# Kernel optimization log

Hardware: AMD Instinct MI355X
Metric: run time of the kernel (lower is better)

Reference implementation:

```python
import jax, jax.numpy as jnp
import numpy as np
import math

N_TERMS = 10
TWO_PI = 2.0 * math.pi


def _zernike_tables(n_terms):
    # Terms in the exact order of the torch loops: n in [0,n_terms), m in range(-n, n+1, 2).
    terms = []
    for n in range(n_terms):
        for m in range(-n, n + 1, 2):
            terms.append((n, m))
    T = len(terms)  # n_terms*(n_terms+1)/2 = 55 for n_terms=10
    C = np.zeros((T, n_terms), dtype=np.float32)  # C[t, p] = coeff of rho**p for term t
    ms = np.zeros(T, dtype=np.float32)
    for t, (n, m) in enumerate(terms):
        am = abs(m)
        for k in range((n - am) // 2 + 1):
            c = ((-1) ** k) * math.factorial(n - k) / (
                math.factorial(k)
                * math.factorial((n + am) // 2 - k)
                * math.factorial((n - am) // 2 - k)
            )
            C[t, n - 2 * k] += c
        ms[t] = m
    return C, ms


_C_NP, _MS_NP = _zernike_tables(N_TERMS)


def setup_inputs() -> dict:
    key = jax.random.key(0)
    x = jax.random.normal(key, (32, 1, 1024, 1024), dtype=jnp.float32)
    return {"x": x}


def reference(x) -> jnp.ndarray:
    # FFT features
    fft_image = jnp.fft.rfft2(x)                    # [B,1,H,Wr], Wr = W//2+1
    magnitude = jnp.abs(fft_image)
    phase = jnp.angle(fft_image)
    pu = jnp.where(phase < 0, phase + TWO_PI, phase)  # "unwrapped" phase

    # Phase gradients (torch.gradient semantics == jnp.gradient: central diff, one-sided edges)
    grad_y, grad_x = jnp.gradient(pu, axis=(2, 3))

    # Zernike coefficients over the phase map grid
    B, _, H, Wr = pu.shape
    yv = jnp.linspace(-1.0, 1.0, H)
    xv = jnp.linspace(-1.0, 1.0, Wr)
    gy, gx = jnp.meshgrid(yv, xv, indexing="ij")   # [H,Wr]
    rho = jnp.sqrt(gx ** 2 + gy ** 2)
    theta = jnp.arctan2(gy, gx)
    mask = (rho <= 1.0).astype(pu.dtype)

    C = jnp.asarray(_C_NP)                          # [T,P]
    ms = jnp.asarray(_MS_NP)                        # [T]
    powers = jnp.arange(N_TERMS, dtype=pu.dtype)    # rho**0 .. rho**(n_terms-1)
    rho_pows = rho[None] ** powers[:, None, None]   # [P,H,Wr]
    R = jnp.einsum("tp,phw->thw", C, rho_pows)     # radial polynomials, [T,H,Wr]
    mt = ms[:, None, None] * theta[None]
    ang = jnp.where(ms[:, None, None] >= 0, jnp.cos(mt), jnp.sin(-mt))
    Z = R * ang                                     # [T,H,Wr]

    pm = pu[:, 0] * mask                            # [B,H,Wr]
    coeffs = jnp.einsum("bhw,thw->bt", pm, Z) / jnp.sum(mask)  # [B,T]

    # Slope stats (torch .std is unbiased -> ddof=1)
    slope_stats = jnp.concatenate(
        [
            grad_x.mean(axis=(2, 3)),
            grad_y.mean(axis=(2, 3)),
            grad_x.std(axis=(2, 3), ddof=1),
            grad_y.std(axis=(2, 3), ddof=1),
        ],
        axis=1,
    )                                               # [B,4]

    freq_features = jnp.max(magnitude, axis=(2, 3))  # [B,1]

    return jnp.concatenate([coeffs, slope_stats, freq_features], axis=1)  # [B,60]
```

## Files before the change

### kernel.cpp

```cpp
#include <hip/hip_runtime.h>
#include <math.h>

#define BATCH 32
#define HH 1024
#define WW 1024
#define WR 513
#define NPIX (HH * WR)
#define TWO_PI_F 6.28318530717958647692f

#define LGKM_SYNC() __asm__ __volatile__("s_waitcnt lgkmcnt(0)" ::: "memory")

__device__ __forceinline__ float2 cadd(float2 a, float2 b) { return make_float2(a.x + b.x, a.y + b.y); }
__device__ __forceinline__ float2 csub(float2 a, float2 b) { return make_float2(a.x - b.x, a.y - b.y); }
__device__ __forceinline__ float2 cmul(float2 a, float2 b) {
    return make_float2(a.x * b.x - a.y * b.y, a.x * b.y + a.y * b.x);
}

__device__ __forceinline__ float fast_atan2f(float y, float x) {
    float ax = __builtin_fabsf(x), ay = __builtin_fabsf(y);
    float mx = fmaxf(ax, ay), mn = fminf(ax, ay);
    float a = mn * __builtin_amdgcn_rcpf(mx);
    float s = a * a;
    float r = fmaf(fmaf(fmaf(fmaf(0.0208351f, s, -0.085133f), s, 0.180141f),
                        s, -0.3302995f), s, 0.999866f) * a;
    if (ay > ax) r = 1.5707963268f - r;
    if (x < 0.0f) r = 3.1415926536f - r;
    return (y < 0.0f) ? -r : r;
}

__device__ __forceinline__ void fft16(float2* d) {
    float2 b[16];
#pragma unroll
    for (int t = 0; t < 4; ++t) {
        float2 x0 = d[t], x1 = d[t + 4], x2 = d[t + 8], x3 = d[t + 12];
        float2 a0 = cadd(x0, x2), a1 = csub(x0, x2), a2 = cadd(x1, x3), a3 = csub(x1, x3);
        b[4 * t + 0] = cadd(a0, a2);
        b[4 * t + 1] = make_float2(a1.x + a3.y, a1.y - a3.x);
        b[4 * t + 2] = csub(a0, a2);
        b[4 * t + 3] = make_float2(a1.x - a3.y, a1.y + a3.x);
    }
    const float2 W1[4] = {make_float2(1.0f, 0.0f),
                          make_float2(0.92387953f, -0.38268343f),
                          make_float2(0.70710678f, -0.70710678f),
                          make_float2(0.38268343f, -0.92387953f)};
#pragma unroll
    for (int t = 0; t < 4; ++t) {
        float2 w1 = W1[t], w2 = cmul(w1, w1), w3 = cmul(w2, w1);
        float2 x0 = b[t], x1 = cmul(b[t + 4], w1), x2 = cmul(b[t + 8], w2), x3 = cmul(b[t + 12], w3);
        float2 a0 = cadd(x0, x2), a1 = csub(x0, x2), a2 = cadd(x1, x3), a3 = csub(x1, x3);
        d[t + 0]  = cadd(a0, a2);
        d[t + 4]  = make_float2(a1.x + a3.y, a1.y - a3.x);
        d[t + 8]  = csub(a0, a2);
        d[t + 12] = make_float2(a1.x - a3.y, a1.y + a3.x);
    }
}

__device__ __forceinline__ void wave_fft1024(float2* v, float* sb, int lane) {
    fft16(v);
    float s, c;
    __sincosf(-TWO_PI_F * (float)lane * (1.0f / 1024.0f), &s, &c);
    float2 T = make_float2(c, s), w = T;
#pragma unroll
    for (int k2 = 1; k2 < 16; ++k2) { v[k2] = cmul(v[k2], w); w = cmul(w, T); }
    const int k2p = lane & 15, qp = lane >> 4;
    float tx[16];
#pragma unroll
    for (int k2 = 0; k2 < 16; ++k2) sb[68 * k2 + lane] = v[k2].x;
    LGKM_SYNC();
#pragma unroll
    for (int m = 0; m < 16; ++m) tx[m] = sb[68 * k2p + 4 * m + qp];
    LGKM_SYNC();
#pragma unroll
    for (int k2 = 0; k2 < 16; ++k2) sb[68 * k2 + lane] = v[k2].y;
    LGKM_SYNC();
#pragma unroll
    for (int m = 0; m < 16; ++m) v[m] = make_float2(tx[m], sb[68 * k2p + 4 * m + qp]);
    LGKM_SYNC();
    fft16(v);
    __sincosf(-TWO_PI_F * (float)qp * (1.0f / 64.0f), &s, &c);
    float2 U = make_float2(c, s);
    w = U;
#pragma unroll
    for (int km = 1; km < 16; ++km) { v[km] = cmul(v[km], w); w = cmul(w, U); }
    const bool hi2 = (lane & 32) != 0, hi1 = (lane & 16) != 0;
#pragma unroll
    for (int m = 0; m < 16; ++m) {
        float2 a = v[m];
        float2 o = make_float2(__shfl_xor(a.x, 32, 64), __shfl_xor(a.y, 32, 64));
        float2 s1 = hi2 ? csub(o, a) : cadd(a, o);
        if (hi2 && hi1) s1 = make_float2(s1.y, -s1.x);
        float2 o2 = make_float2(__shfl_xor(s1.x, 16, 64), __shfl_xor(s1.y, 16, 64));
        v[m] = hi1 ? csub(o2, s1) : cadd(s1, o2);
    }
}

__global__ __launch_bounds__(256, 4) void row_fft_kernel(const float* __restrict__ x,
                                                         float2* __restrict__ rf2) {
    __shared__ float2 buf[4 * 1088];
    const int t = threadIdx.x, w = t >> 6, lane = t & 63;
    const int b = blockIdx.x >> 7;
    const int h0 = (blockIdx.x & 127) * 8;
    const float* r0 = x + ((long long)b * HH + h0 + 2 * w) * (long long)WW;
    const float* r1 = r0 + WW;
    float2 v[16];
#pragma unroll
    for (int j = 0; j < 16; ++j) v[j] = make_float2(r0[lane + 64 * j], r1[lane + 64 * j]);
    float2* mybuf = buf + w * 1088;
    wave_fft1024(v, (float*)mybuf, lane);
    const int kq = 2 * ((lane >> 4) & 1) + ((lane >> 5) & 1);
    const int kbase = (lane & 15) + 256 * kq;
#pragma unroll
    for (int m = 0; m < 16; ++m) mybuf[kbase + 16 * m] = v[m];
    __syncthreads();
    for (int idx = t; idx < 513 * 8; idx += 256) {
        int k = idx >> 3, j = idx & 7, p = j >> 1, which = j & 1;
        float2 zk = buf[p * 1088 + k];
        float2 zn = buf[p * 1088 + ((1024 - k) & 1023)];
        float2 val = which ? make_float2(0.5f * (zk.y + zn.y), 0.5f * (zn.x - zk.x))
                           : make_float2(0.5f * (zk.x + zn.x), 0.5f * (zk.y - zn.y));
        rf2[((long long)b * WR + k) * 1024 + h0 + j] = val;
    }
}

__global__ __launch_bounds__(128, 4) void col_fft_kernel(float2* __restrict__ rf2,
                                                         float* __restrict__ magmax) {
    __shared__ float sb[2 * 1088];
    const int t = threadIdx.x, w = t >> 6, lane = t & 63;
    const int fid = blockIdx.x * 2 + w;
    const int b = fid / WR, k = fid - b * WR;
    float2* row = rf2 + ((long long)b * WR + k) * 1024;
    float2 v[16];
#pragma unroll
    for (int j = 0; j < 16; ++j) v[j] = row[lane + 64 * j];
    wave_fft1024(v, sb + w * 1088, lane);
    float* pu = (float*)row;
    const int kq = 2 * ((lane >> 4) & 1) + ((lane >> 5) & 1);
    const int hbase = (lane & 15) + 256 * kq;
    float mmax = 0.0f;
#pragma unroll
    for (int m = 0; m < 16; ++m) {
        float2 z = v[m];
        mmax = fmaxf(mmax, __builtin_amdgcn_sqrtf(z.x * z.x + z.y * z.y));
        float ph = fast_atan2f(z.y, z.x);
        pu[hbase + 16 * m] = (ph < 0.0f) ? ph + TWO_PI_F : ph;
    }
#pragma unroll
    for (int off = 32; off; off >>= 1) mmax = fmaxf(mmax, __shfl_down(mmax, off));
    if (lane == 0) atomicMax((int*)(magmax + b), __float_as_int(mmax));
}

#define WRED(var, idx)                                                     \
    {                                                                      \
        float r_ = var;                                                    \
        _Pragma("unroll")                                                  \
        for (int off_ = 32; off_; off_ >>= 1) r_ += __shfl_down(r_, off_); \
        if (lane == 0) red[wv * 64 + (idx)] = r_;                          \
    }

__global__ __launch_bounds__(256, 2) void stats_kernel(float* __restrict__ pu) {
    __shared__ float red[4 * 64];
    const int b = blockIdx.y;
    const int k0 = blockIdx.x * 9;
    const float* base = pu + (long long)b * WR * 2048;
    float a00 = 0.f, a11 = 0.f, a20 = 0.f, a22 = 0.f, a31 = 0.f, a33 = 0.f,
          a40 = 0.f, a42 = 0.f, a44 = 0.f, a51 = 0.f, a53 = 0.f, a55 = 0.f,
          a60 = 0.f, a62 = 0.f, a64 = 0.f, a66 = 0.f, a71 = 0.f, a73 = 0.f,
          a75 = 0.f, a77 = 0.f, a80 = 0.f, a82 = 0.f, a84 = 0.f, a86 = 0.f,
          a88 = 0.f, a91 = 0.f, a93 = 0.f, a95 = 0.f, a97 = 0.f, a99 = 0.f;
    float b11 = 0.f, b22 = 0.f, b31 = 0.f, b33 = 0.f, b42 = 0.f, b44 = 0.f,
          b51 = 0.f, b53 = 0.f, b55 = 0.f, b62 = 0.f, b64 = 0.f, b66 = 0.f,
          b71 = 0.f, b73 = 0.f, b75 = 0.f, b77 = 0.f, b82 = 0.f, b84 = 0.f,
          b86 = 0.f, b88 = 0.f, b91 = 0.f, b93 = 0.f, b95 = 0.f, b97 = 0.f,
          b99 = 0.f;
    float sgx = 0.f, sgx2 = 0.f, sgy = 0.f, sgy2 = 0.f, cnt = 0.f;

    for (int kk = 0; kk < 9; ++kk) {
        const int k = k0 + kk;
        const float* rowc = base + (long long)k * 2048;
        const float* rowm = rowc - 2048;
        const float* rowp = rowc + 2048;
        const float xv = -1.0f + (1.0f / 256.0f) * (float)k;
        const float xv2 = xv * xv;
        for (int h = threadIdx.x; h < 1024; h += 256) {
            float v = rowc[h];
            float gx, gy;
            if (k == 0)            gx = rowp[h] - v;
            else if (k == WR - 1)  gx = v - rowm[h];
            else                   gx = 0.5f * (rowp[h] - rowm[h]);
            if (h == 0)            gy = rowc[1] - v;
            else if (h == 1023)    gy = v - rowc[1022];
            else                   gy = 0.5f * (rowc[h + 1] - rowc[h - 1]);
            sgx += gx; sgx2 += gx * gx; sgy += gy; sgy2 += gy * gy;

            const float yv = -1.0f + (2.0f / 1023.0f) * (float)h;
            const float r2 = xv2 + yv * yv;
            if (r2 <= 1.0f) {
                cnt += 1.0f;
                const float rho = sqrtf(r2);
                const float inv = rsqrtf(r2);
                const float c1 = xv * inv;
                const float s1 = yv * inv;
                const float c2 = 2.f * c1 * c1 - 1.f;
                const float c3 = 2.f * c1 * c2 - c1;
                const float c4 = 2.f * c1 * c3 - c2;
                const float c5 = 2.f * c1 * c4 - c3;
                const float c6 = 2.f * c1 * c5 - c4;
                const float c7 = 2.f * c1 * c6 - c5;
                const float c8 = 2.f * c1 * c7 - c6;
                const float c9 = 2.f * c1 * c8 - c7;
                const float s2 = 2.f * c1 * s1;
                const float s3 = 2.f * c1 * s2 - s1;
                const float s4 = 2.f * c1 * s3 - s2;
                const float s5 = 2.f * c1 * s4 - s3;
                const float s6 = 2.f * c1 * s5 - s4;
                const float s7 = 2.f * c1 * s6 - s5;
                const float s8 = 2.f * c1 * s7 - s6;
                const float s9 = 2.f * c1 * s8 - s7;
                const float w0 = v,        w1 = w0 * rho, w2 = w1 * rho, w3 = w2 * rho,
                            w4 = w3 * rho, w5 = w4 * rho, w6 = w5 * rho, w7 = w6 * rho,
                            w8 = w7 * rho, w9 = w8 * rho;
                a00 += w0;
                a11 += w1 * c1;
                a20 += w2;      a22 += w2 * c2;
                a31 += w3 * c1; a33 += w3 * c3;
                a40 += w4;      a42 += w4 * c2; a44 += w4 * c4;
                a51 += w5 * c1; a53 += w5 * c3; a55 += w5 * c5;
                a60 += w6;      a62 += w6 * c2; a64 += w6 * c4; a66 += w6 * c6;
                a71 += w7 * c1; a73 += w7 * c3; a75 += w7 * c5; a77 += w7 * c7;
                a80 += w8;      a82 += w8 * c2; a84 += w8 * c4; a86 += w8 * c6; a88 += w8 * c8;
                a91 += w9 * c1; a93 += w9 * c3; a95 += w9 * c5; a97 += w9 * c7; a99 += w9 * c9;
                b11 += w1 * s1;
                b22 += w2 * s2;
                b31 += w3 * s1; b33 += w3 * s3;
                b42 += w4 * s2; b44 += w4 * s4;
                b51 += w5 * s1; b53 += w5 * s3; b55 += w5 * s5;
                b62 += w6 * s2; b64 += w6 * s4; b66 += w6 * s6;
                b71 += w7 * s1; b73 += w7 * s3; b75 += w7 * s5; b77 += w7 * s7;
                b82 += w8 * s2; b84 += w8 * s4; b86 += w8 * s6; b88 += w8 * s8;
                b91 += w9 * s1; b93 += w9 * s3; b95 += w9 * s5; b97 += w9 * s7; b99 += w9 * s9;
            }
        }
    }

    const int wv = threadIdx.x >> 6, lane = threadIdx.x & 63;
    WRED(a00, 0);  WRED(a11, 1);  WRED(a20, 2);  WRED(a22, 3);  WRED(a31, 4);
    WRED(a33, 5);  WRED(a40, 6);  WRED(a42, 7);  WRED(a44, 8);  WRED(a51, 9);
    WRED(a53, 10); WRED(a55, 11); WRED(a60, 12); WRED(a62, 13); WRED(a64, 14);
    WRED(a66, 15); WRED(a71, 16); WRED(a73, 17); WRED(a75, 18); WRED(a77, 19);
    WRED(a80, 20); WRED(a82, 21); WRED(a84, 22); WRED(a86, 23); WRED(a88, 24);
    WRED(a91, 25); WRED(a93, 26); WRED(a95, 27); WRED(a97, 28); WRED(a99, 29);
    WRED(b11, 30); WRED(b22, 31); WRED(b31, 32); WRED(b33, 33); WRED(b42, 34);
    WRED(b44, 35); WRED(b51, 36); WRED(b53, 37); WRED(b55, 38); WRED(b62, 39);
    WRED(b64, 40); WRED(b66, 41); WRED(b71, 42); WRED(b73, 43); WRED(b75, 44);
    WRED(b77, 45); WRED(b82, 46); WRED(b84, 47); WRED(b86, 48); WRED(b88, 49);
    WRED(b91, 50); WRED(b93, 51); WRED(b95, 52); WRED(b97, 53); WRED(b99, 54);
    WRED(sgx, 55); WRED(sgx2, 56); WRED(sgy, 57); WRED(sgy2, 58); WRED(cnt, 59);
    __syncthreads();
    const int t = threadIdx.x;
    if (t < 60) {
        float s = red[t] + red[64 + t] + red[128 + t] + red[192 + t];
        pu[((long long)(b * 57 + blockIdx.x)) * 2048 + 1024 + t] = s;
    }
}

__device__ int moment_index(int p, int a, int is_cos) {
    int ai = 0;
    for (int pp = 0; pp < 10; ++pp)
        for (int aa = (pp & 1); aa <= pp; aa += 2) {
            if (is_cos && pp == p && aa == a) return ai;
            ++ai;
        }
    for (int pp = 1; pp < 10; ++pp)
        for (int aa = ((pp & 1) ? 1 : 2); aa <= pp; aa += 2) {
            if (!is_cos && pp == p && aa == a) return ai;
            ++ai;
        }
    return 0;
}

__device__ float factf(int n) {
    float f = 1.0f;
    for (int i = 2; i <= n; ++i) f *= (float)i;
    return f;
}

__global__ void finalize_kernel(const float* __restrict__ pu,
                                const float* __restrict__ magmax,
                                float* __restrict__ out) {
    __shared__ float abf[64];
    const int b = blockIdx.x;
    const int j = threadIdx.x;
    if (j < 60) {
        float s = 0.0f;
        for (int i = 0; i < 57; ++i)
            s += pu[((long long)(b * 57 + i)) * 2048 + 1024 + j];
        abf[j] = s;
    }
    __syncthreads();
    if (j >= 60) return;
    const float NF = (float)NPIX;
    float val;
    if (j < 55) {
        int tt = j, n = 0;
        while (tt >= n + 1) { tt -= (n + 1); ++n; }
        int m = -n + 2 * tt;
        int am = m < 0 ? -m : m;
        float s = 0.0f;
        for (int k = 0; k <= (n - am) / 2; ++k) {
            float c = factf(n - k) /
                      (factf(k) * factf((n + am) / 2 - k) * factf((n - am) / 2 - k));
            if (k & 1) c = -c;
            int p = n - 2 * k;
            s += c * abf[moment_index(p, am, m >= 0 ? 1 : 0)];
        }
        val = s / abf[59];
    } else if (j == 55) {
        val = abf[55] / NF;
    } else if (j == 56) {
        val = abf[57] / NF;
    } else if (j == 57) {
        float sum = abf[55], sq = abf[56];
        val = sqrtf(fmaxf(0.0f, (sq - sum * sum / NF) / (NF - 1.0f)));
    } else if (j == 58) {
        float sum = abf[57], sq = abf[58];
        val = sqrtf(fmaxf(0.0f, (sq - sum * sum / NF) / (NF - 1.0f)));
    } else {
        val = magmax[b];
    }
    out[b * 60 + j] = val;
}

extern "C" void kernel_launch(void* const* d_in, const int* in_sizes, int n_in,
                              void* d_out, int out_size, void* d_ws, size_t ws_size,
                              hipStream_t stream) {
    (void)in_sizes; (void)n_in; (void)out_size; (void)ws_size;
    const float* x = (const float*)d_in[0];
    float* out = (float*)d_out;

    float* magmax = (float*)d_ws;
    float2* rf2 = (float2*)((char*)d_ws + 16384);

    hipMemsetAsync(d_ws, 0, 16384, stream);
    row_fft_kernel<<<BATCH * 128, 256, 0, stream>>>(x, rf2);
    col_fft_kernel<<<(BATCH * WR) / 2, 128, 0, stream>>>(rf2, magmax);
    dim3 gridC(57, BATCH);
    stats_kernel<<<gridC, 256, 0, stream>>>((float*)rf2);
    finalize_kernel<<<BATCH, 64, 0, stream>>>((const float*)rf2, magmax, out);
}
```

Measured before the change: 509.1 us.

## Fuse Zernike moments and y-gradient stats into column FFT kernel

Computes the phase-map Zernike moments, y-gradient sums and mask count directly inside the column FFT kernel. The unwrapped phase is staged in padded shared memory and reduced per wave, and the per-row partials are written into the spare half of each row. The old stats kernel becomes a lighter float4-vectorized x-gradient kernel, and finalize sums 513 per-row partials instead of 57. This avoids re-reading the phase map for the moment computation but raises register pressure in the FFT kernel and makes finalize's serial loop longer.

```diff
diff --git a/kernel.cpp b/kernel.cpp
--- a/kernel.cpp
+++ b/kernel.cpp
@@ -9,6 +9,8 @@
 #define TWO_PI_F 6.28318530717958647692f
 
 #define LGKM_SYNC() __asm__ __volatile__("s_waitcnt lgkmcnt(0)" ::: "memory")
+
+#define PUIDX(h) ((h) + (((h) >> 8) << 3))
 
 __device__ __forceinline__ float2 cadd(float2 a, float2 b) { return make_float2(a.x + b.x, a.y + b.y); }
 __device__ __forceinline__ float2 csub(float2 a, float2 b) { return make_float2(a.x - b.x, a.y - b.y); }
@@ -132,7 +134,9 @@
     float2 v[16];
 #pragma unroll
     for (int j = 0; j < 16; ++j) v[j] = row[lane + 64 * j];
-    wave_fft1024(v, sb + w * 1088, lane);
+    float* mysb = sb + w * 1088;
+    wave_fft1024(v, mysb, lane);
+
     float* pu = (float*)row;
     const int kq = 2 * ((lane >> 4) & 1) + ((lane >> 5) & 1);
     const int hbase = (lane & 15) + 256 * kq;
@@ -142,26 +146,18 @@
         float2 z = v[m];
         mmax = fmaxf(mmax, __builtin_amdgcn_sqrtf(z.x * z.x + z.y * z.y));
         float ph = fast_atan2f(z.y, z.x);
-        pu[hbase + 16 * m] = (ph < 0.0f) ? ph + TWO_PI_F : ph;
+        float p = (ph < 0.0f) ? ph + TWO_PI_F : ph;
+        const int h = hbase + 16 * m;
+        pu[h] = p;
+        mysb[PUIDX(h)] = p;
     }
 #pragma unroll
     for (int off = 32; off; off >>= 1) mmax = fmaxf(mmax, __shfl_down(mmax, off));
     if (lane == 0) atomicMax((int*)(magmax + b), __float_as_int(mmax));
-}
-
-#define WRED(var, idx)                                                     \
-    {                                                                      \
-        float r_ = var;                                                    \
-        _Pragma("unroll")                                                  \
-        for (int off_ = 32; off_; off_ >>= 1) r_ += __shfl_down(r_, off_); \
-        if (lane == 0) red[wv * 64 + (idx)] = r_;                          \
-    }
-
-__global__ __launch_bounds__(256, 2) void stats_kernel(float* __restrict__ pu) {
-    __shared__ float red[4 * 64];
-    const int b = blockIdx.y;
-    const int k0 = blockIdx.x * 9;
-    const float* base = pu + (long long)b * WR * 2048;
+    LGKM_SYNC();
+
+    const float xv = -1.0f + (1.0f / 256.0f) * (float)k;
+    const float xv2 = xv * xv;
     float a00 = 0.f, a11 = 0.f, a20 = 0.f, a22 = 0.f, a31 = 0.f, a33 = 0.f,
           a40 = 0.f, a42 = 0.f, a44 = 0.f, a51 = 0.f, a53 = 0.f, a55 = 0.f,
           a60 = 0.f, a62 = 0.f, a64 = 0.f, a66 = 0.f, a71 = 0.f, a73 = 0.f,
@@ -172,94 +168,131 @@
           b71 = 0.f, b73 = 0.f, b75 = 0.f, b77 = 0.f, b82 = 0.f, b84 = 0.f,
           b86 = 0.f, b88 = 0.f, b91 = 0.f, b93 = 0.f, b95 = 0.f, b97 = 0.f,
           b99 = 0.f;
-    float sgx = 0.f, sgx2 = 0.f, sgy = 0.f, sgy2 = 0.f, cnt = 0.f;
-
+    float sgy = 0.f, sgy2 = 0.f, cnt = 0.f;
+
+#pragma unroll
+    for (int m = 0; m < 16; ++m) {
+        const int h = hbase + 16 * m;
+        const float v0 = mysb[PUIDX(h)];
+        float gy;
+        if (h == 0)         gy = mysb[PUIDX(1)] - v0;
+        else if (h == 1023) gy = v0 - mysb[PUIDX(1022)];
+        else                gy = 0.5f * (mysb[PUIDX(h + 1)] - mysb[PUIDX(h - 1)]);
+        sgy += gy; sgy2 += gy * gy;
+
+        const float yv = -1.0f + (2.0f / 1023.0f) * (float)h;
+        const float r2 = xv2 + yv * yv;
+        if (r2 <= 1.0f) {
+            cnt += 1.0f;
+            const float rho = sqrtf(r2);
+            const float inv = rsqrtf(r2);
+            const float c1 = xv * inv;
+            const float s1 = yv * inv;
+            const float c2 = 2.f * c1 * c1 - 1.f;
+            const float c3 = 2.f * c1 * c2 - c1;
+            const float c4 = 2.f * c1 * c3 - c2;
+            const float c5 = 2.f * c1 * c4 - c3;
+            const float c6 = 2.f * c1 * c5 - c4;
+            const float c7 = 2.f * c1 * c6 - c5;
+            const float c8 = 2.f * c1 * c7 - c6;
+            const float c9 = 2.f * c1 * c8 - c7;
+            const float s2 = 2.f * c1 * s1;
+            const float s3 = 2.f * c1 * s2 - s1;
+            const float s4 = 2.f * c1 * s3 - s2;
+            const float s5 = 2.f * c1 * s4 - s3;
+            const float s6 = 2.f * c1 * s5 - s4;
+            const float s7 = 2.f * c1 * s6 - s5;
+            const float s8 = 2.f * c1 * s7 - s6;
+            const float s9 = 2.f * c1 * s8 - s7;
+            const float w0 = v0,       w1 = w0 * rho, w2 = w1 * rho, w3 = w2 * rho,
+                        w4 = w3 * rho, w5 = w4 * rho, w6 = w5 * rho, w7 = w6 * rho,
+                        w8 = w7 * rho, w9 = w8 * rho;
+            a00 += w0;
+            a11 += w1 * c1;
+            a20 += w2;      a22 += w2 * c2;
+            a31 += w3 * c1; a33 += w3 * c3;
+            a40 += w4;      a42 += w4 * c2; a44 += w4 * c4;
+            a51 += w5 * c1; a53 += w5 * c3; a55 += w5 * c5;
+            a60 += w6;      a62 += w6 * c2; a64 += w6 * c4; a66 += w6 * c6;
+            a71 += w7 * c1; a73 += w7 * c3; a75 += w7 * c5; a77 += w7 * c7;
+            a80 += w8;      a82 += w8 * c2; a84 += w8 * c4; a86 += w8 * c6; a88 += w8 * c8;
+            a91 += w9 * c1; a93 += w9 * c3; a95 += w9 * c5; a97 += w9 * c7; a99 += w9 * c9;
+            b11 += w1 * s1;
+            b22 += w2 * s2;
+            b31 += w3 * s1; b33 += w3 * s3;
+            b42 += w4 * s2; b44 += w4 * s4;
+            b51 += w5 * s1; b53 += w5 * s3; b55 += w5 * s5;
+            b62 += w6 * s2; b64 += w6 * s4; b66 += w6 * s6;
+            b71 += w7 * s1; b73 += w7 * s3; b75 += w7 * s5; b77 += w7 * s7;
+            b82 += w8 * s2; b84 += w8 * s4; b86 += w8 * s6; b88 += w8 * s8;
+            b91 += w9 * s1; b93 += w9 * s3; b95 += w9 * s5; b97 += w9 * s7; b99 += w9 * s9;
+        }
+    }
+    LGKM_SYNC();
+
+#define CWRED(var, idx)                                                     \
+    {                                                                       \
+        float r_ = var;                                                     \
+        _Pragma("unroll")                                                   \
+        for (int off_ = 32; off_; off_ >>= 1) r_ += __shfl_down(r_, off_);  \
+        if (lane == 0) mysb[(idx)] = r_;                                    \
+    }
+    CWRED(a00, 0);  CWRED(a11, 1);  CWRED(a20, 2);  CWRED(a22, 3);  CWRED(a31, 4);
+    CWRED(a33, 5);  CWRED(a40, 6);  CWRED(a42, 7);  CWRED(a44, 8);  CWRED(a51, 9);
+    CWRED(a53, 10); CWRED(a55, 11); CWRED(a60, 12); CWRED(a62, 13); CWRED(a64, 14);
+    CWRED(a66, 15); CWRED(a71, 16); CWRED(a73, 17); CWRED(a75, 18); CWRED(a77, 19);
+    CWRED(a80, 20); CWRED(a82, 21); CWRED(a84, 22); CWRED(a86, 23); CWRED(a88, 24);
+    CWRED(a91, 25); CWRED(a93, 26); CWRED(a95, 27); CWRED(a97, 28); CWRED(a99, 29);
+    CWRED(b11, 30); CWRED(b22, 31); CWRED(b31, 32); CWRED(b33, 33); CWRED(b42, 34);
+    CWRED(b44, 35); CWRED(b51, 36); CWRED(b53, 37); CWRED(b55, 38); CWRED(b62, 39);
+    CWRED(b64, 40); CWRED(b66, 41); CWRED(b71, 42); CWRED(b73, 43); CWRED(b75, 44);
+    CWRED(b77, 45); CWRED(b82, 46); CWRED(b84, 47); CWRED(b86, 48); CWRED(b88, 49);
+    CWRED(b91, 50); CWRED(b93, 51); CWRED(b95, 52); CWRED(b97, 53); CWRED(b99, 54);
+    CWRED(sgy, 55); CWRED(sgy2, 56); CWRED(cnt, 57);
+#undef CWRED
+    LGKM_SYNC();
+    if (lane < 58) pu[1024 + lane] = mysb[lane];
+}
+
+__global__ __launch_bounds__(256, 2) void gx_kernel(float* __restrict__ pu) {
+    __shared__ float red[2 * 4];
+    const int b = blockIdx.y;
+    const int k0 = blockIdx.x * 9;
+    float* base = pu + (long long)b * WR * 2048;
+    const int t = threadIdx.x;
+    float sgx = 0.f, sgx2 = 0.f;
     for (int kk = 0; kk < 9; ++kk) {
         const int k = k0 + kk;
         const float* rowc = base + (long long)k * 2048;
-        const float* rowm = rowc - 2048;
-        const float* rowp = rowc + 2048;
-        const float xv = -1.0f + (1.0f / 256.0f) * (float)k;
-        const float xv2 = xv * xv;
-        for (int h = threadIdx.x; h < 1024; h += 256) {
-            float v = rowc[h];
-            float gx, gy;
-            if (k == 0)            gx = rowp[h] - v;
-            else if (k == WR - 1)  gx = v - rowm[h];
-            else                   gx = 0.5f * (rowp[h] - rowm[h]);
-            if (h == 0)            gy = rowc[1] - v;
-            else if (h == 1023)    gy = v - rowc[1022];
-            else                   gy = 0.5f * (rowc[h + 1] - rowc[h - 1]);
-            sgx += gx; sgx2 += gx * gx; sgy += gy; sgy2 += gy * gy;
-
-            const float yv = -1.0f + (2.0f / 1023.0f) * (float)h;
-            const float r2 = xv2 + yv * yv;
-            if (r2 <= 1.0f) {
-                cnt += 1.0f;
-                const float rho = sqrtf(r2);
-                const float inv = rsqrtf(r2);
-                const float c1 = xv * inv;
-                const float s1 = yv * inv;
-                const float c2 = 2.f * c1 * c1 - 1.f;
-                const float c3 = 2.f * c1 * c2 - c1;
-                const float c4 = 2.f * c1 * c3 - c2;
-                const float c5 = 2.f * c1 * c4 - c3;
-                const float c6 = 2.f * c1 * c5 - c4;
-                const float c7 = 2.f * c1 * c6 - c5;
-                const float c8 = 2.f * c1 * c7 - c6;
-                const float c9 = 2.f * c1 * c8 - c7;
-                const float s2 = 2.f * c1 * s1;
-                const float s3 = 2.f * c1 * s2 - s1;
-                const float s4 = 2.f * c1 * s3 - s2;
-                const float s5 = 2.f * c1 * s4 - s3;
-                const float s6 = 2.f * c1 * s5 - s4;
-                const float s7 = 2.f * c1 * s6 - s5;
-                const float s8 = 2.f * c1 * s7 - s6;
-                const float s9 = 2.f * c1 * s8 - s7;
-                const float w0 = v,        w1 = w0 * rho, w2 = w1 * rho, w3 = w2 * rho,
-                            w4 = w3 * rho, w5 = w4 * rho, w6 = w5 * rho, w7 = w6 * rho,
-                            w8 = w7 * rho, w9 = w8 * rho;
-                a00 += w0;
-                a11 += w1 * c1;
-                a20 += w2;      a22 += w2 * c2;
-                a31 += w3 * c1; a33 += w3 * c3;
-                a40 += w4;      a42 += w4 * c2; a44 += w4 * c4;
-                a51 += w5 * c1; a53 += w5 * c3; a55 += w5 * c5;
-                a60 += w6;      a62 += w6 * c2; a64 += w6 * c4; a66 += w6 * c6;
-                a71 += w7 * c1; a73 += w7 * c3; a75 += w7 * c5; a77 += w7 * c7;
-                a80 += w8;      a82 += w8 * c2; a84 += w8 * c4; a86 += w8 * c6; a88 += w8 * c8;
-                a91 += w9 * c1; a93 += w9 * c3; a95 += w9 * c5; a97 += w9 * c7; a99 += w9 * c9;
-                b11 += w1 * s1;
-                b22 += w2 * s2;
-                b31 += w3 * s1; b33 += w3 * s3;
-                b42 += w4 * s2; b44 += w4 * s4;
-                b51 += w5 * s1; b53 += w5 * s3; b55 += w5 * s5;
-                b62 += w6 * s2; b64 += w6 * s4; b66 += w6 * s6;
-                b71 += w7 * s1; b73 += w7 * s3; b75 += w7 * s5; b77 += w7 * s7;
-                b82 += w8 * s2; b84 += w8 * s4; b86 += w8 * s6; b88 += w8 * s8;
-                b91 += w9 * s1; b93 += w9 * s3; b95 += w9 * s5; b97 += w9 * s7; b99 += w9 * s9;
-            }
-        }
-    }
-
-    const int wv = threadIdx.x >> 6, lane = threadIdx.x & 63;
-    WRED(a00, 0);  WRED(a11, 1);  WRED(a20, 2);  WRED(a22, 3);  WRED(a31, 4);
-    WRED(a33, 5);  WRED(a40, 6);  WRED(a42, 7);  WRED(a44, 8);  WRED(a51, 9);
-    WRED(a53, 10); WRED(a55, 11); WRED(a60, 12); WRED(a62, 13); WRED(a64, 14);
-    WRED(a66, 15); WRED(a71, 16); WRED(a73, 17); WRED(a75, 18); WRED(a77, 19);
-    WRED(a80, 20); WRED(a82, 21); WRED(a84, 22); WRED(a86, 23); WRED(a88, 24);
-    WRED(a91, 25); WRED(a93, 26); WRED(a95, 27); WRED(a97, 28); WRED(a99, 29);
-    WRED(b11, 30); WRED(b22, 31); WRED(b31, 32); WRED(b33, 33); WRED(b42, 34);
-    WRED(b44, 35); WRED(b51, 36); WRED(b53, 37); WRED(b55, 38); WRED(b62, 39);
-    WRED(b64, 40); WRED(b66, 41); WRED(b71, 42); WRED(b73, 43); WRED(b75, 44);
-    WRED(b77, 45); WRED(b82, 46); WRED(b84, 47); WRED(b86, 48); WRED(b88, 49);
-    WRED(b91, 50); WRED(b93, 51); WRED(b95, 52); WRED(b97, 53); WRED(b99, 54);
-    WRED(sgx, 55); WRED(sgx2, 56); WRED(sgy, 57); WRED(sgy2, 58); WRED(cnt, 59);
+        float4 g4;
+        if (k == 0) {
+            float4 c4 = *(const float4*)(rowc + 4 * t);
+            float4 p4 = *(const float4*)(rowc + 2048 + 4 * t);
+            g4 = make_float4(p4.x - c4.x, p4.y - c4.y, p4.z - c4.z, p4.w - c4.w);
+        } else if (k == WR - 1) {
+            float4 c4 = *(const float4*)(rowc + 4 * t);
+            float4 m4 = *(const float4*)(rowc - 2048 + 4 * t);
+            g4 = make_float4(c4.x - m4.x, c4.y - m4.y, c4.z - m4.z, c4.w - m4.w);
+        } else {
+            float4 p4 = *(const float4*)(rowc + 2048 + 4 * t);
+            float4 m4 = *(const float4*)(rowc - 2048 + 4 * t);
+            g4 = make_float4(0.5f * (p4.x - m4.x), 0.5f * (p4.y - m4.y),
+                             0.5f * (p4.z - m4.z), 0.5f * (p4.w - m4.w));
+        }
+        sgx += g4.x + g4.y + g4.z + g4.w;
+        sgx2 += g4.x * g4.x + g4.y * g4.y + g4.z * g4.z + g4.w * g4.w;
+    }
+    const int wv = t >> 6, lane = t & 63;
+#pragma unroll
+    for (int off = 32; off; off >>= 1) sgx += __shfl_down(sgx, off);
+#pragma unroll
+    for (int off = 32; off; off >>= 1) sgx2 += __shfl_down(sgx2, off);
+    if (lane == 0) { red[wv] = sgx; red[4 + wv] = sgx2; }
     __syncthreads();
-    const int t = threadIdx.x;
-    if (t < 60) {
-        float s = red[t] + red[64 + t] + red[128 + t] + red[192 + t];
-        pu[((long long)(b * 57 + blockIdx.x)) * 2048 + 1024 + t] = s;
+    if (t == 0) {
+        float* dst = base + (long long)k0 * 2048 + 1100;
+        dst[0] = red[0] + red[1] + red[2] + red[3];
+        dst[1] = red[4] + red[5] + red[6] + red[7];
     }
 }
 
@@ -290,11 +323,22 @@
     __shared__ float abf[64];
     const int b = blockIdx.x;
     const int j = threadIdx.x;
-    if (j < 60) {
+    const float* base = pu + (long long)b * WR * 2048;
+    if (j < 58) {
+        float s = 0.0f;
+        for (int i = 0; i < WR; ++i)
+            s += base[(long long)i * 2048 + 1024 + j];
+        abf[j] = s;
+    } else if (j == 58) {
         float s = 0.0f;
         for (int i = 0; i < 57; ++i)
-            s += pu[((long long)(b * 57 + i)) * 2048 + 1024 + j];
-        abf[j] = s;
+            s += base[(long long)(i * 9) * 2048 + 1100];
+        abf[58] = s;
+    } else if (j == 59) {
+        float s = 0.0f;
+        for (int i = 0; i < 57; ++i)
+            s += base[(long long)(i * 9) * 2048 + 1101];
+        abf[59] = s;
     }
     __syncthreads();
     if (j >= 60) return;
@@ -313,16 +357,16 @@
             int p = n - 2 * k;
             s += c * abf[moment_index(p, am, m >= 0 ? 1 : 0)];
         }
-        val = s / abf[59];
+        val = s / abf[57];
     } else if (j == 55) {
+        val = abf[58] / NF;
+    } else if (j == 56) {
         val = abf[55] / NF;
-    } else if (j == 56) {
-        val = abf[57] / NF;
     } else if (j == 57) {
-        float sum = abf[55], sq = abf[56];
+        float sum = abf[58], sq = abf[59];
         val = sqrtf(fmaxf(0.0f, (sq - sum * sum / NF) / (NF - 1.0f)));
     } else if (j == 58) {
-        float sum = abf[57], sq = abf[58];
+        float sum = abf[55], sq = abf[56];
         val = sqrtf(fmaxf(0.0f, (sq - sum * sum / NF) / (NF - 1.0f)));
     } else {
         val = magmax[b];
@@ -340,10 +384,10 @@
     float* magmax = (float*)d_ws;
     float2* rf2 = (float2*)((char*)d_ws + 16384);
 
-    hipMemsetAsync(d_ws, 0, 16384, stream);
+    (void)hipMemsetAsync(d_ws, 0, 16384, stream);
     row_fft_kernel<<<BATCH * 128, 256, 0, stream>>>(x, rf2);
     col_fft_kernel<<<(BATCH * WR) / 2, 128, 0, stream>>>(rf2, magmax);
-    dim3 gridC(57, BATCH);
-    stats_kernel<<<gridC, 256, 0, stream>>>((float*)rf2);
+    dim3 gridG(57, BATCH);
+    gx_kernel<<<gridG, 256, 0, stream>>>((float*)rf2);
     finalize_kernel<<<BATCH, 64, 0, stream>>>((const float*)rf2, magmax, out);
 }
```

New measurement: 523.7 us. 1.03x slower.
